# Performance work log

Hardware: AMD Instinct MI355X
Metric: run time of the kernel (lower is better)

## Reference

```python
import jax, jax.numpy as jnp
import numpy as np

B, S, I, H = 32, 1024, 512, 512


def setup_inputs() -> dict:
    key = jax.random.key(0)
    ks = jax.random.split(key, 5)
    scale_ih = 1.0 / np.sqrt(I)
    scale_hh = 1.0 / np.sqrt(H)
    return {
        "x": jax.random.normal(ks[0], (B, S, I), dtype=jnp.float32),
        "W_ih": jax.random.normal(ks[1], (4 * H, I), dtype=jnp.float32) * scale_ih,
        "W_hh": jax.random.normal(ks[2], (4 * H, H), dtype=jnp.float32) * scale_hh,
        "b_ih": jax.random.normal(ks[3], (4 * H,), dtype=jnp.float32) * scale_hh,
        "b_hh": jax.random.normal(ks[4], (4 * H,), dtype=jnp.float32) * scale_hh,
        "h0": jnp.zeros((B, H), dtype=jnp.float32),
        "c0": jnp.zeros((B, H), dtype=jnp.float32),
    }


def reference(x, W_ih, W_hh, b_ih, b_hh, h0, c0):
    # Precompute input contribution for all timesteps: [B, S, 4H]
    x_gates = jnp.einsum('bsi,gi->bsg', x, W_ih) + b_ih + b_hh

    def step(carry, xg_t):
        h, c = carry
        gates = xg_t + h @ W_hh.T  # [B, 4H]
        i_g, f_g, g_g, o_g = jnp.split(gates, 4, axis=-1)
        i_g = jax.nn.sigmoid(i_g)
        f_g = jax.nn.sigmoid(f_g)
        g_g = jnp.tanh(g_g)
        o_g = jax.nn.sigmoid(o_g)
        c_new = f_g * c + i_g * g_g
        h_new = o_g * jnp.tanh(c_new)
        return (h_new, c_new), h_new

    # scan over time: [S, B, 4H]
    (h_n, c_n), ys = jax.lax.scan(step, (h0, c0), jnp.swapaxes(x_gates, 0, 1))
    output = jnp.swapaxes(ys, 0, 1)  # [B, S, H]
    return output, h_n, c_n
```

## Files before the change

### kernel.cpp

```cpp
#include <hip/hip_runtime.h>
#include <stdint.h>


typedef __attribute__((ext_vector_type(8))) short bf16x8;
typedef __attribute__((ext_vector_type(4))) float f32x4;

__device__ __forceinline__ unsigned short f2bf(float f) {
  union { float f; unsigned u; } v; v.f = f;
  unsigned r = (v.u + 0x7fffu + ((v.u >> 16) & 1u)) >> 16;
  return (unsigned short)r;
}
__device__ __forceinline__ float bf2f(unsigned short h) {
  union { unsigned u; float f; } v; v.u = ((unsigned)h) << 16;
  return v.f;
}

__global__ __launch_bounds__(256) void cvt_bf16(const float* __restrict__ in,
                                                unsigned short* __restrict__ out, int n) {
  int i = (blockIdx.x * 256 + threadIdx.x) * 4;
  if (i >= n) return;
  float4 v = *(const float4*)(in + i);
  ushort4 o;
  o.x = f2bf(v.x); o.y = f2bf(v.y); o.z = f2bf(v.z); o.w = f2bf(v.w);
  *(ushort4*)(out + i) = o;
}

__global__ __launch_bounds__(256) void gemm_xg(const unsigned short* __restrict__ A,
                                               const unsigned short* __restrict__ Bw,
                                               const float* __restrict__ b_ih,
                                               const float* __restrict__ b_hh,
                                               unsigned short* __restrict__ xg) {
  __shared__ unsigned short Asub[128][32];
  __shared__ unsigned short Bsub[128][32];
  const int tid = threadIdx.x;
  const int mb = blockIdx.x >> 4;
  const int nb = blockIdx.x & 15;
  const int wv = tid >> 6, ln = tid & 63;
  const int wr = wv >> 1, wc = wv & 1;
  const int lrow = tid >> 1;
  const int lseg = (tid & 1) * 16;

  const unsigned short* Ag = A + (size_t)(mb * 128 + lrow) * 512 + lseg;
  const unsigned short* Bg = Bw + (size_t)(nb * 128 + lrow) * 512 + lseg;

  f32x4 acc[4][4] = {};
  const int frow = ln & 15;
  const int kq = (ln >> 4) * 8;

  for (int k0 = 0; k0 < 512; k0 += 32) {
    uint4 a0 = *(const uint4*)(Ag + k0);
    uint4 a1 = *(const uint4*)(Ag + k0 + 8);
    uint4 b0 = *(const uint4*)(Bg + k0);
    uint4 b1 = *(const uint4*)(Bg + k0 + 8);
    __syncthreads();
    *(uint4*)&Asub[lrow][lseg]     = a0;
    *(uint4*)&Asub[lrow][lseg + 8] = a1;
    *(uint4*)&Bsub[lrow][lseg]     = b0;
    *(uint4*)&Bsub[lrow][lseg + 8] = b1;
    __syncthreads();
    bf16x8 af[4], bfr[4];
#pragma unroll
    for (int mi = 0; mi < 4; ++mi)
      af[mi] = *(const bf16x8*)&Asub[wr * 64 + mi * 16 + frow][kq];
#pragma unroll
    for (int ni = 0; ni < 4; ++ni)
      bfr[ni] = *(const bf16x8*)&Bsub[wc * 64 + ni * 16 + frow][kq];
#pragma unroll
    for (int mi = 0; mi < 4; ++mi)
#pragma unroll
      for (int ni = 0; ni < 4; ++ni)
        acc[mi][ni] = __builtin_amdgcn_mfma_f32_16x16x32_bf16(af[mi], bfr[ni], acc[mi][ni], 0, 0, 0);
  }

  const int col0 = nb * 128 + wc * 64 + frow;
  float bias[4];
#pragma unroll
  for (int ni = 0; ni < 4; ++ni)
    bias[ni] = b_ih[col0 + ni * 16] + b_hh[col0 + ni * 16];

#pragma unroll
  for (int mi = 0; mi < 4; ++mi) {
    const int m0 = mb * 128 + wr * 64 + mi * 16 + (ln >> 4) * 4;
#pragma unroll
    for (int ni = 0; ni < 4; ++ni) {
#pragma unroll
      for (int rr = 0; rr < 4; ++rr) {
        float v = acc[mi][ni][rr] + bias[ni];
        xg[(size_t)(m0 + rr) * 2048 + col0 + ni * 16] = f2bf(v);
      }
    }
  }
}

__global__ __launch_bounds__(256, 1) void lstm_rec(const unsigned short* __restrict__ xg,
                                                   const float* __restrict__ W_hh,
                                                   const float* __restrict__ h0,
                                                   const float* __restrict__ c0,
                                                   float* __restrict__ out,
                                                   float* __restrict__ hn,
                                                   float* __restrict__ cn,
                                                   float* h_buf,
                                                   unsigned int* cnt) {
  __shared__ float h_lds[2048];
  __shared__ float scratch[64 * 17];
  __shared__ float gates_lds[64 * 5];
  __shared__ float c_lds[64];

  const int tid = threadIdx.x;
  const int g = blockIdx.x >> 5;
  const int w = blockIdx.x & 31;
  const int gb0 = g * 4;
  const int kc = tid >> 6;
  const int r = tid & 63;
  const int grow = (r >> 4) * 512 + w * 16 + (r & 15);
  const int kcb = kc * 128;
  unsigned int* my_cnt = cnt + g * 64;

  float W[128];
  {
    const float* wp = W_hh + (size_t)grow * 512 + kcb;
#pragma unroll
    for (int i = 0; i < 128; i += 4) {
      float4 v = *(const float4*)(wp + i);
      W[i] = v.x; W[i + 1] = v.y; W[i + 2] = v.z; W[i + 3] = v.w;
    }
  }
#pragma unroll
  for (int i = 0; i < 128; ++i) asm volatile("" : "+v"(W[i]));

  {
    const float* hp = h0 + gb0 * 512 + tid * 8;
    float4 va = *(const float4*)hp;
    float4 vb = *(const float4*)(hp + 4);
    *(float4*)&h_lds[tid * 8] = va;
    *(float4*)&h_lds[tid * 8 + 4] = vb;
    if (tid < 64) {
      int jj = tid & 15, bb = tid >> 4;
      c_lds[bb * 16 + jj] = c0[(gb0 + bb) * 512 + w * 16 + jj];
    }
  }
  __syncthreads();

  for (int t = 0; t < 1024; ++t) {
    float xg_v = bf2f(xg[(size_t)((gb0 + kc) * 1024 + t) * 2048 + grow]);

    float acc0 = 0.f, acc1 = 0.f, acc2 = 0.f, acc3 = 0.f;
#pragma unroll
    for (int i = 0; i < 128; i += 4) {
      float4 ha = *(const float4*)&h_lds[kcb + i];
      float4 hb = *(const float4*)&h_lds[512 + kcb + i];
      float4 hc = *(const float4*)&h_lds[1024 + kcb + i];
      float4 hd = *(const float4*)&h_lds[1536 + kcb + i];
      acc0 = fmaf(W[i], ha.x, acc0); acc0 = fmaf(W[i + 1], ha.y, acc0);
      acc0 = fmaf(W[i + 2], ha.z, acc0); acc0 = fmaf(W[i + 3], ha.w, acc0);
      acc1 = fmaf(W[i], hb.x, acc1); acc1 = fmaf(W[i + 1], hb.y, acc1);
      acc1 = fmaf(W[i + 2], hb.z, acc1); acc1 = fmaf(W[i + 3], hb.w, acc1);
      acc2 = fmaf(W[i], hc.x, acc2); acc2 = fmaf(W[i + 1], hc.y, acc2);
      acc2 = fmaf(W[i + 2], hc.z, acc2); acc2 = fmaf(W[i + 3], hc.w, acc2);
      acc3 = fmaf(W[i], hd.x, acc3); acc3 = fmaf(W[i + 1], hd.y, acc3);
      acc3 = fmaf(W[i + 2], hd.z, acc3); acc3 = fmaf(W[i + 3], hd.w, acc3);
    }
    scratch[r * 17 + kc] = acc0;
    scratch[r * 17 + 4 + kc] = acc1;
    scratch[r * 17 + 8 + kc] = acc2;
    scratch[r * 17 + 12 + kc] = acc3;
    __syncthreads();

    {
      float s = xg_v + scratch[r * 17 + kc * 4] + scratch[r * 17 + kc * 4 + 1]
                     + scratch[r * 17 + kc * 4 + 2] + scratch[r * 17 + kc * 4 + 3];
      gates_lds[r * 5 + kc] = s;
    }
    __syncthreads();

    if (tid < 64) {
      const int jj = tid & 15, bb = tid >> 4;
      float gi = gates_lds[jj * 5 + bb];
      float gf = gates_lds[(16 + jj) * 5 + bb];
      float gc = gates_lds[(32 + jj) * 5 + bb];
      float go = gates_lds[(48 + jj) * 5 + bb];
      float ig = 1.f / (1.f + __expf(-gi));
      float fg = 1.f / (1.f + __expf(-gf));
      float gt = tanhf(gc);
      float og = 1.f / (1.f + __expf(-go));
      float c = fmaf(fg, c_lds[bb * 16 + jj], ig * gt);
      c_lds[bb * 16 + jj] = c;
      float hv = og * tanhf(c);
      out[(size_t)((gb0 + bb) * 1024 + t) * 512 + w * 16 + jj] = hv;
      __hip_atomic_store(&h_buf[((t + 1) & 1) * 16384 + (gb0 + bb) * 512 + w * 16 + jj], hv,
                         __ATOMIC_RELAXED, __HIP_MEMORY_SCOPE_AGENT);
      if (t == 1023) {
        hn[(gb0 + bb) * 512 + w * 16 + jj] = hv;
        cn[(gb0 + bb) * 512 + w * 16 + jj] = c;
      }
    }
    __syncthreads();

    if (t < 1023) {
      if (tid == 0) {
        __hip_atomic_fetch_add(my_cnt, 1u, __ATOMIC_RELAXED, __HIP_MEMORY_SCOPE_AGENT);
        const unsigned target = 32u * (unsigned)(t + 1);
        while (__hip_atomic_load(my_cnt, __ATOMIC_RELAXED, __HIP_MEMORY_SCOPE_AGENT) < target)
          __builtin_amdgcn_s_sleep(2);
      }
      __syncthreads();
      const unsigned long long* hb =
          (const unsigned long long*)(h_buf + ((t + 1) & 1) * 16384 + gb0 * 512 + tid * 8);
      unsigned long long v[4];
#pragma unroll
      for (int q = 0; q < 4; ++q)
        v[q] = __hip_atomic_load(hb + q, __ATOMIC_RELAXED, __HIP_MEMORY_SCOPE_AGENT);
#pragma unroll
      for (int q = 0; q < 4; ++q)
        *(unsigned long long*)&h_lds[tid * 8 + q * 2] = v[q];
      __syncthreads();
    }
  }
}

extern "C" void kernel_launch(void* const* d_in, const int* in_sizes, int n_in,
                              void* d_out, int out_size, void* d_ws, size_t ws_size,
                              hipStream_t stream) {
  const float* x    = (const float*)d_in[0];
  const float* W_ih = (const float*)d_in[1];
  const float* W_hh = (const float*)d_in[2];
  const float* b_ih = (const float*)d_in[3];
  const float* b_hh = (const float*)d_in[4];
  const float* h0   = (const float*)d_in[5];
  const float* c0   = (const float*)d_in[6];
  float* out = (float*)d_out;
  float* hn = out + (size_t)32 * 1024 * 512;
  float* cn = hn + 32 * 512;

  uint8_t* ws = (uint8_t*)d_ws;
  unsigned short* xg   = (unsigned short*)ws;
  unsigned short* x_bf = (unsigned short*)(ws + 134217728u);
  unsigned short* w_bf = (unsigned short*)(ws + 167772160u);
  float* h_buf         = (float*)(ws + 169869312u);
  unsigned int* cnt    = (unsigned int*)(ws + 170000384u);

  hipMemsetAsync(cnt, 0, 8 * 256, stream);
  cvt_bf16<<<dim3(16384), dim3(256), 0, stream>>>(x, x_bf, 16777216);
  cvt_bf16<<<dim3(1024), dim3(256), 0, stream>>>(W_ih, w_bf, 1048576);
  gemm_xg<<<dim3(4096), dim3(256), 0, stream>>>(x_bf, w_bf, b_ih, b_hh, xg);

  void* args[] = {(void*)&xg, (void*)&W_hh, (void*)&h0, (void*)&c0,
                  (void*)&out, (void*)&hn, (void*)&cn, (void*)&h_buf, (void*)&cnt};
  hipLaunchCooperativeKernel((const void*)lstm_rec, dim3(256), dim3(256), args, 0, stream);
}
```

Measured before the change: 3.880 ms.

## Double recurrent block threads to split K dimension eight ways

Launches the recurrent LSTM kernel with 512 threads per block instead of 256, so each thread holds 64 W_hh weights in registers and covers a 64-wide slice of the hidden vector instead of 128. The partial sums are reduced across eight K-chunks through a reorganized scratch layout, and the h reload is spread across more threads. This halves the serial per-thread dot-product length on each timestep's critical path, at the cost of an extra reduction step and more threads taking part in each barrier.

```diff
diff --git a/kernel.cpp b/kernel.cpp
--- a/kernel.cpp
+++ b/kernel.cpp
@@ -92,7 +92,7 @@
   }
 }
 
-__global__ __launch_bounds__(256, 1) void lstm_rec(const unsigned short* __restrict__ xg,
+__global__ __launch_bounds__(512, 1) void lstm_rec(const unsigned short* __restrict__ xg,
                                                    const float* __restrict__ W_hh,
                                                    const float* __restrict__ h0,
                                                    const float* __restrict__ c0,
@@ -102,7 +102,7 @@
                                                    float* h_buf,
                                                    unsigned int* cnt) {
   __shared__ float h_lds[2048];
-  __shared__ float scratch[64 * 17];
+  __shared__ float scratch[2048];
   __shared__ float gates_lds[64 * 5];
   __shared__ float c_lds[64];
 
@@ -113,27 +113,23 @@
   const int kc = tid >> 6;
   const int r = tid & 63;
   const int grow = (r >> 4) * 512 + w * 16 + (r & 15);
-  const int kcb = kc * 128;
+  const int kcb = kc * 64;
   unsigned int* my_cnt = cnt + g * 64;
 
-  float W[128];
+  float W[64];
   {
     const float* wp = W_hh + (size_t)grow * 512 + kcb;
 #pragma unroll
-    for (int i = 0; i < 128; i += 4) {
+    for (int i = 0; i < 64; i += 4) {
       float4 v = *(const float4*)(wp + i);
       W[i] = v.x; W[i + 1] = v.y; W[i + 2] = v.z; W[i + 3] = v.w;
     }
   }
 #pragma unroll
-  for (int i = 0; i < 128; ++i) asm volatile("" : "+v"(W[i]));
+  for (int i = 0; i < 64; ++i) asm volatile("" : "+v"(W[i]));
 
   {
-    const float* hp = h0 + gb0 * 512 + tid * 8;
-    float4 va = *(const float4*)hp;
-    float4 vb = *(const float4*)(hp + 4);
-    *(float4*)&h_lds[tid * 8] = va;
-    *(float4*)&h_lds[tid * 8 + 4] = vb;
+    *(float4*)&h_lds[tid * 4] = *(const float4*)(h0 + gb0 * 512 + tid * 4);
     if (tid < 64) {
       int jj = tid & 15, bb = tid >> 4;
       c_lds[bb * 16 + jj] = c0[(gb0 + bb) * 512 + w * 16 + jj];
@@ -141,12 +137,17 @@
   }
   __syncthreads();
 
+  const int rr = tid & 63, bb2 = tid >> 6;
+  const int grow_r = (rr >> 4) * 512 + w * 16 + (rr & 15);
+
   for (int t = 0; t < 1024; ++t) {
-    float xg_v = bf2f(xg[(size_t)((gb0 + kc) * 1024 + t) * 2048 + grow]);
+    float xg_v = 0.f;
+    if (tid < 256)
+      xg_v = bf2f(xg[(size_t)((gb0 + bb2) * 1024 + t) * 2048 + grow_r]);
 
     float acc0 = 0.f, acc1 = 0.f, acc2 = 0.f, acc3 = 0.f;
 #pragma unroll
-    for (int i = 0; i < 128; i += 4) {
+    for (int i = 0; i < 64; i += 4) {
       float4 ha = *(const float4*)&h_lds[kcb + i];
       float4 hb = *(const float4*)&h_lds[512 + kcb + i];
       float4 hc = *(const float4*)&h_lds[1024 + kcb + i];
@@ -160,16 +161,18 @@
       acc3 = fmaf(W[i], hd.x, acc3); acc3 = fmaf(W[i + 1], hd.y, acc3);
       acc3 = fmaf(W[i + 2], hd.z, acc3); acc3 = fmaf(W[i + 3], hd.w, acc3);
     }
-    scratch[r * 17 + kc] = acc0;
-    scratch[r * 17 + 4 + kc] = acc1;
-    scratch[r * 17 + 8 + kc] = acc2;
-    scratch[r * 17 + 12 + kc] = acc3;
-    __syncthreads();
-
-    {
-      float s = xg_v + scratch[r * 17 + kc * 4] + scratch[r * 17 + kc * 4 + 1]
-                     + scratch[r * 17 + kc * 4 + 2] + scratch[r * 17 + kc * 4 + 3];
-      gates_lds[r * 5 + kc] = s;
+    scratch[0 * 512 + kc * 64 + r] = acc0;
+    scratch[1 * 512 + kc * 64 + r] = acc1;
+    scratch[2 * 512 + kc * 64 + r] = acc2;
+    scratch[3 * 512 + kc * 64 + r] = acc3;
+    __syncthreads();
+
+    if (tid < 256) {
+      const float* sp = &scratch[bb2 * 512 + rr];
+      float s = xg_v;
+#pragma unroll
+      for (int q = 0; q < 8; ++q) s += sp[q * 64];
+      gates_lds[rr * 5 + bb2] = s;
     }
     __syncthreads();
 
@@ -205,14 +208,11 @@
       }
       __syncthreads();
       const unsigned long long* hb =
-          (const unsigned long long*)(h_buf + ((t + 1) & 1) * 16384 + gb0 * 512 + tid * 8);
-      unsigned long long v[4];
-#pragma unroll
-      for (int q = 0; q < 4; ++q)
-        v[q] = __hip_atomic_load(hb + q, __ATOMIC_RELAXED, __HIP_MEMORY_SCOPE_AGENT);
-#pragma unroll
-      for (int q = 0; q < 4; ++q)
-        *(unsigned long long*)&h_lds[tid * 8 + q * 2] = v[q];
+          (const unsigned long long*)(h_buf + ((t + 1) & 1) * 16384 + gb0 * 512 + tid * 4);
+      unsigned long long v0 = __hip_atomic_load(hb,     __ATOMIC_RELAXED, __HIP_MEMORY_SCOPE_AGENT);
+      unsigned long long v1 = __hip_atomic_load(hb + 1, __ATOMIC_RELAXED, __HIP_MEMORY_SCOPE_AGENT);
+      *(unsigned long long*)&h_lds[tid * 4]     = v0;
+      *(unsigned long long*)&h_lds[tid * 4 + 2] = v1;
       __syncthreads();
     }
   }
@@ -246,5 +246,5 @@
 
   void* args[] = {(void*)&xg, (void*)&W_hh, (void*)&h0, (void*)&c0,
                   (void*)&out, (void*)&hn, (void*)&cn, (void*)&h_buf, (void*)&cnt};
-  hipLaunchCooperativeKernel((const void*)lstm_rec, dim3(256), dim3(256), args, 0, stream);
-}
+  hipLaunchCooperativeKernel((const void*)lstm_rec, dim3(256), dim3(512), args, 0, stream);
+}
```

Measured after the change: 3.388 ms. 1.15x faster.
